# Kernel tuning notes

Measured on AMD Instinct MI355X. Metric: run time of the kernel, lower is better.

## Reference

```python
import jax, jax.numpy as jnp
import numpy as np

N, E, DIN, DOUT, H = 50000, 800000, 256, 128, 8
DH = DOUT // H  # per-head dim = 16


def setup_inputs() -> dict:
    key = jax.random.key(0)
    k1, k2, k3, k4, k5 = jax.random.split(key, 5)
    x = jax.random.normal(k1, (N, DIN), dtype=jnp.float32)
    edge_index = jax.random.randint(k2, (2, E), 0, N)
    W_trans = jax.random.normal(k3, (DOUT, DIN), dtype=jnp.float32) / np.sqrt(DIN).astype(np.float32)
    W_att = jax.random.normal(k4, (1, 2 * DH), dtype=jnp.float32) / np.sqrt(2 * DH).astype(np.float32)
    b_att = jax.random.normal(k5, (1,), dtype=jnp.float32) * 0.01
    return {"x": x, "W_trans": W_trans, "W_att": W_att, "b_att": b_att, "edge_index": edge_index}


def reference(x, W_trans, W_att, b_att, edge_index):
    n = x.shape[0]
    # append self-loops (as in the torch module)
    loops = jnp.arange(n, dtype=edge_index.dtype)
    ei = jnp.concatenate([edge_index, jnp.stack([loops, loops])], axis=1)  # [2, E+N]
    src, dst = ei[0], ei[1]

    # linear transform, split heads: [n, H, DH]
    h = (x @ W_trans.T).reshape(n, H, DH)
    h_i = h[src]  # [Etot, H, DH]
    h_j = h[dst]  # [Etot, H, DH]

    # per-edge attention score: concat -> linear -> leaky_relu(0.2)
    s = jnp.concatenate([h_i, h_j], axis=-1) @ W_att.T + b_att  # [Etot, H, 1]
    s = jnp.where(s >= 0, s, 0.2 * s)

    # softmax(dim=0)*exp_sum/scatter_add(exp) == exp(s)/segment_sum(exp(s)) per dst node
    e = jnp.exp(s)
    denom = jax.ops.segment_sum(e, dst, num_segments=n)  # [n, H, 1]
    att = e / denom[dst]

    out = jax.ops.segment_sum(h_i * att, dst, num_segments=n)  # [n, H, DH]
    return out.reshape(n, DOUT)  # head_fusion='cat'
```

## Files before the change

kernel.cpp:

```cpp
#include <hip/hip_runtime.h>


constexpr int DIN  = 256;
constexpr int DOUT = 128;
constexpr int H    = 8;
constexpr int CAP  = 5120;
constexpr int CHUNK = 1024;

typedef __attribute__((ext_vector_type(8))) short bf16x8;
typedef __attribute__((ext_vector_type(4))) float f32x4;

__device__ __forceinline__ float lrelu(float s) { return s >= 0.0f ? s : 0.2f * s; }

__device__ __forceinline__ unsigned short f2bf(float f) {
  unsigned u = __float_as_uint(f);
  u += 0x7FFF + ((u >> 16) & 1);
  return (unsigned short)(u >> 16);
}
__device__ __forceinline__ float bflo(unsigned u) { return __uint_as_float(u << 16); }
__device__ __forceinline__ float bfhi(unsigned u) { return __uint_as_float(u & 0xFFFF0000u); }

__device__ __forceinline__ int wave_incl_scan(int v, int lane) {
#pragma unroll
  for (int d = 1; d < 64; d <<= 1) {
    int t = __shfl_up(v, d, 64);
    if (lane >= d) v += t;
  }
  return v;
}

__global__ void conv_w(const float* __restrict__ W, unsigned short* __restrict__ Wbf,
                       int n, int* __restrict__ bcount, int nb) {
  int i = blockIdx.x * blockDim.x + threadIdx.x;
  if (i < n) Wbf[i] = f2bf(W[i]);
  if (blockIdx.x == 0 && threadIdx.x < nb) bcount[threadIdx.x] = 0;
}

__global__ __launch_bounds__(256) void bp_gemm(const float* __restrict__ x,
                                               const unsigned short* __restrict__ Wbf,
                                               unsigned short* __restrict__ hbf, int N,
                                               const int* __restrict__ ei,
                                               int* __restrict__ bcount,
                                               unsigned* __restrict__ pair_buf,
                                               int E, int nb, int bp_blocks) {
  __shared__ int hist[256];
  __shared__ int gbase[256];
  if ((int)blockIdx.x < bp_blocks) {
    int c0 = blockIdx.x * CHUNK;
    hist[threadIdx.x] = 0;
    __syncthreads();
    int dcache[4];
#pragma unroll
    for (int q = 0; q < 4; ++q) {
      int e = c0 + q * 256 + threadIdx.x;
      dcache[q] = (e < E) ? ei[E + e] : -1;
      if (dcache[q] >= 0) atomicAdd(&hist[dcache[q] >> 8], 1);
    }
    __syncthreads();
    if (threadIdx.x < nb) {
      int c = hist[threadIdx.x];
      gbase[threadIdx.x] = c ? atomicAdd(&bcount[threadIdx.x], c) : 0;
    }
    __syncthreads();
    hist[threadIdx.x] = 0;
    __syncthreads();
#pragma unroll
    for (int q = 0; q < 4; ++q) {
      int e = c0 + q * 256 + threadIdx.x;
      if (dcache[q] >= 0) {
        int s = ei[e];
        int bk = dcache[q] >> 8;
        int r = atomicAdd(&hist[bk], 1);
        pair_buf[bk * CAP + gbase[bk] + r] = ((unsigned)s << 8) | (unsigned)(dcache[q] & 255);
      }
    }
    return;
  }
  int gb = blockIdx.x - bp_blocks;
  int tid = threadIdx.x;
  int w = tid >> 6, lane = tid & 63;
  int mr = lane & 15, kg = lane >> 4;
  int m0 = gb * 32 + (w >> 1) * 16;
  int nt0 = (w & 1) * 4;
  if (m0 >= N) return;
  int rr = m0 + mr;
  if (rr >= N) rr = N - 1;
  const float* xrow = x + (size_t)rr * DIN + kg * 8;

  float4 xa[8], xc[8];
#pragma unroll
  for (int ks = 0; ks < 8; ++ks) {
    xa[ks] = *(const float4*)(xrow + ks * 32);
    xc[ks] = *(const float4*)(xrow + ks * 32 + 4);
  }

  f32x4 acc[4];
#pragma unroll
  for (int t = 0; t < 4; ++t) acc[t] = (f32x4){0.f, 0.f, 0.f, 0.f};

#pragma unroll
  for (int ks = 0; ks < 8; ++ks) {
    bf16x8 a;
    a[0] = (short)f2bf(xa[ks].x); a[1] = (short)f2bf(xa[ks].y);
    a[2] = (short)f2bf(xa[ks].z); a[3] = (short)f2bf(xa[ks].w);
    a[4] = (short)f2bf(xc[ks].x); a[5] = (short)f2bf(xc[ks].y);
    a[6] = (short)f2bf(xc[ks].z); a[7] = (short)f2bf(xc[ks].w);
#pragma unroll
    for (int t = 0; t < 4; ++t) {
      bf16x8 b = *(const bf16x8*)(Wbf + ((nt0 + t) * 16 + mr) * DIN + ks * 32 + kg * 8);
      acc[t] = __builtin_amdgcn_mfma_f32_16x16x32_bf16(a, b, acc[t], 0, 0, 0);
    }
  }
#pragma unroll
  for (int t = 0; t < 4; ++t) {
#pragma unroll
    for (int r = 0; r < 4; ++r) {
      int row = m0 + kg * 4 + r;
      if (row < N) hbf[row * DOUT + (nt0 + t) * 16 + mr] = f2bf(acc[t][r]);
    }
  }
}

__global__ __launch_bounds__(256) void fs_ns(const unsigned* __restrict__ pair_buf,
                                             const int* __restrict__ bcount,
                                             int* __restrict__ offsets,
                                             unsigned short* __restrict__ src_sorted,
                                             const unsigned short* __restrict__ hbf,
                                             const float* __restrict__ Wa,
                                             float* __restrict__ a_src,
                                             float* __restrict__ a_dst,
                                             int N, int E, int nb) {
  __shared__ int cnt[256];
  __shared__ int cur[256];
  __shared__ int redS[256];
  __shared__ int wsumS[4];
  const int t = threadIdx.x;
  if ((int)blockIdx.x >= nb) {
    int idx = ((int)blockIdx.x - nb) * 256 + t;
    if (idx >= N * H) return;
    int v = idx >> 3, hh = idx & 7;
    const unsigned short* hp = hbf + (size_t)v * DOUT + hh * 16;
    uint4 p0 = *(const uint4*)hp;
    uint4 p1 = *(const uint4*)(hp + 8);
    float hv[16];
    hv[0] = bflo(p0.x); hv[1] = bfhi(p0.x); hv[2] = bflo(p0.y); hv[3] = bfhi(p0.y);
    hv[4] = bflo(p0.z); hv[5] = bfhi(p0.z); hv[6] = bflo(p0.w); hv[7] = bfhi(p0.w);
    hv[8] = bflo(p1.x); hv[9] = bfhi(p1.x); hv[10] = bflo(p1.y); hv[11] = bfhi(p1.y);
    hv[12] = bflo(p1.z); hv[13] = bfhi(p1.z); hv[14] = bflo(p1.w); hv[15] = bfhi(p1.w);
    float s1 = 0.f, s2 = 0.f;
#pragma unroll
    for (int d = 0; d < 16; ++d) {
      s1 += hv[d] * Wa[d];
      s2 += hv[d] * Wa[16 + d];
    }
    a_src[idx] = s1;
    a_dst[idx] = s2;
    return;
  }
  const int B = blockIdx.x;
  const int node0 = B * 256;
  const int v = node0 + t;
  const int valid = (v < N);
  cnt[t] = valid ? 1 : 0;
  __syncthreads();
  const int cntE = bcount[B];
  const unsigned* reg = pair_buf + B * CAP;
  for (int i = t; i < cntE; i += 256)
    atomicAdd(&cnt[reg[i] & 255], 1);
  redS[t] = (t < B) ? bcount[t] : 0;
  __syncthreads();
  for (int s = 128; s > 0; s >>= 1) {
    if (t < s) redS[t] += redS[t + s];
    __syncthreads();
  }
  const int csr_base = redS[0] + node0;
  int val = cnt[t];
  int lane = t & 63, wv = t >> 6;
  int inc = wave_incl_scan(val, lane);
  if (lane == 63) wsumS[wv] = inc;
  __syncthreads();
  int base = 0;
  for (int q = 0; q < wv; ++q) base += wsumS[q];
  int ex = base + inc - val;
  cur[t] = ex + 1;
  if (valid) {
    offsets[v] = csr_base + ex;
    src_sorted[csr_base + ex] = (unsigned short)v;
  }
  if (B == 0 && t == 0) offsets[N] = E + N;
  __syncthreads();
  for (int i = t; i < cntE; i += 256) {
    unsigned p = reg[i];
    int k = atomicAdd(&cur[p & 255], 1);
    src_sorted[csr_base + k] = (unsigned short)(p >> 8);
  }
}

__global__ __launch_bounds__(256) void aggregate(const unsigned short* __restrict__ hbf,
                                                 const float* __restrict__ a_src,
                                                 const float* __restrict__ a_dst,
                                                 const float* __restrict__ b_att,
                                                 const int* __restrict__ offsets,
                                                 const unsigned short* __restrict__ src_sorted,
                                                 float* __restrict__ out, int N) {
  int wid = blockIdx.x * 4 + (threadIdx.x >> 6);
  if (wid >= N) return;
  int lane = threadIdx.x & 63;
  int g = lane >> 4, sl = lane & 15;
  int head = sl >> 1;
  float adv = a_dst[wid * H + head] + b_att[0];
  int beg = offsets[wid], end = offsets[wid + 1];
  float a0 = 0, a1 = 0, a2 = 0, a3 = 0, a4 = 0, a5 = 0, a6 = 0, a7 = 0, den = 0;
  for (int j0 = beg; j0 < end; j0 += 4) {
    int jj = j0 + g;
    bool valid = jj < end;
    int jc = valid ? jj : beg;
    int s = src_sorted[jc];
    float as = a_src[s * H + head];
    uint4 u = *(const uint4*)(hbf + s * DOUT + sl * 8);
    float e = valid ? __expf(lrelu(as + adv)) : 0.f;
    den += e;
    a0 += e * bflo(u.x); a1 += e * bfhi(u.x);
    a2 += e * bflo(u.y); a3 += e * bfhi(u.y);
    a4 += e * bflo(u.z); a5 += e * bfhi(u.z);
    a6 += e * bflo(u.w); a7 += e * bfhi(u.w);
  }
  den += __shfl_xor(den, 16, 64); den += __shfl_xor(den, 32, 64);
  a0 += __shfl_xor(a0, 16, 64); a0 += __shfl_xor(a0, 32, 64);
  a1 += __shfl_xor(a1, 16, 64); a1 += __shfl_xor(a1, 32, 64);
  a2 += __shfl_xor(a2, 16, 64); a2 += __shfl_xor(a2, 32, 64);
  a3 += __shfl_xor(a3, 16, 64); a3 += __shfl_xor(a3, 32, 64);
  a4 += __shfl_xor(a4, 16, 64); a4 += __shfl_xor(a4, 32, 64);
  a5 += __shfl_xor(a5, 16, 64); a5 += __shfl_xor(a5, 32, 64);
  a6 += __shfl_xor(a6, 16, 64); a6 += __shfl_xor(a6, 32, 64);
  a7 += __shfl_xor(a7, 16, 64); a7 += __shfl_xor(a7, 32, 64);
  float inv = 1.0f / den;
  if (g == 0) {
    float4 o = make_float4(a0 * inv, a1 * inv, a2 * inv, a3 * inv);
    *(float4*)&out[wid * DOUT + sl * 8] = o;
  } else if (g == 1) {
    float4 o = make_float4(a4 * inv, a5 * inv, a6 * inv, a7 * inv);
    *(float4*)&out[wid * DOUT + sl * 8 + 4] = o;
  }
}

extern "C" void kernel_launch(void* const* d_in, const int* in_sizes, int n_in,
                              void* d_out, int out_size, void* d_ws, size_t ws_size,
                              hipStream_t stream) {
  const float* x     = (const float*)d_in[0];
  const float* W     = (const float*)d_in[1];
  const float* Wa    = (const float*)d_in[2];
  const float* b_att = (const float*)d_in[3];
  const int*   ei    = (const int*)d_in[4];
  const int N  = in_sizes[0] / DIN;
  const int E  = in_sizes[4] / 2;
  const int NB = (N + 255) / 256;
  float* out = (float*)d_out;

  char* p = (char*)d_ws;
  auto take = [&p](size_t bytes) {
    uintptr_t u = ((uintptr_t)p + 15) & ~(uintptr_t)15;
    p = (char*)(u + bytes);
    return (void*)u;
  };
  unsigned short* hbf = (unsigned short*)take((size_t)N * DOUT * 2);
  unsigned short* Wbf = (unsigned short*)take((size_t)DOUT * DIN * 2);
  float* a_src        = (float*)take((size_t)N * H * 4);
  float* a_dst        = (float*)take((size_t)N * H * 4);
  int* bcount         = (int*)take((size_t)NB * 4);
  unsigned* pair_buf  = (unsigned*)take((size_t)NB * CAP * 4);
  int* offsets        = (int*)take((size_t)(N + 1) * 4);
  unsigned short* src_sorted = (unsigned short*)take((size_t)(E + N + 16) * 2);

  dim3 b256(256);
  const int bp_blocks   = (E + CHUNK - 1) / CHUNK;
  const int gemm_blocks = (N + 31) / 32;
  const int ns_blocks   = (N * H + 255) / 256;

  conv_w<<<dim3((DOUT * DIN + 255) / 256), b256, 0, stream>>>(W, Wbf, DOUT * DIN, bcount, NB);
  bp_gemm<<<dim3(bp_blocks + gemm_blocks), b256, 0, stream>>>(
      x, Wbf, hbf, N, ei, bcount, pair_buf, E, NB, bp_blocks);
  fs_ns<<<dim3(NB + ns_blocks), b256, 0, stream>>>(
      pair_buf, bcount, offsets, src_sorted, hbf, Wa, a_src, a_dst, N, E, NB);
  aggregate<<<dim3((N + 3) / 4), b256, 0, stream>>>(hbf, a_src, a_dst, b_att, offsets,
                                                    src_sorted, out, N);
}
```

Before: 202.5 us.

## Drop weight-conversion kernel, convert W inline, enlarge bucket chunks, reorder fused blocks

Removes the separate conv_w launch: the GEMM now reads fp32 W directly and converts it to bf16 in registers, and the bucket counters are cleared with hipMemsetAsync instead. The edge-bucketing chunk grows from 1024 to 4096 edges per block, which cuts the number of global atomics on bucket counts. Block order in the fused kernels is swapped so GEMM blocks and node-score blocks are dispatched first. The trade-off is twice the W bytes loaded per GEMM block, extra conversion ALU work, and fewer, larger bucketing blocks that hold more registers.

```diff
diff --git a/kernel.cpp b/kernel.cpp
--- a/kernel.cpp
+++ b/kernel.cpp
@@ -1,11 +1,12 @@
 #include <hip/hip_runtime.h>
+#include <string.h>
 
 
 constexpr int DIN  = 256;
 constexpr int DOUT = 128;
 constexpr int H    = 8;
 constexpr int CAP  = 5120;
-constexpr int CHUNK = 1024;
+constexpr int CHUNK = 4096;
 
 typedef __attribute__((ext_vector_type(8))) short bf16x8;
 typedef __attribute__((ext_vector_type(4))) float f32x4;
@@ -29,29 +30,31 @@
   return v;
 }
 
-__global__ void conv_w(const float* __restrict__ W, unsigned short* __restrict__ Wbf,
-                       int n, int* __restrict__ bcount, int nb) {
-  int i = blockIdx.x * blockDim.x + threadIdx.x;
-  if (i < n) Wbf[i] = f2bf(W[i]);
-  if (blockIdx.x == 0 && threadIdx.x < nb) bcount[threadIdx.x] = 0;
-}
-
-__global__ __launch_bounds__(256) void bp_gemm(const float* __restrict__ x,
-                                               const unsigned short* __restrict__ Wbf,
+__device__ __forceinline__ bf16x8 pack8(const float4& lo, const float4& hi) {
+  bf16x8 a;
+  a[0] = (short)f2bf(lo.x); a[1] = (short)f2bf(lo.y);
+  a[2] = (short)f2bf(lo.z); a[3] = (short)f2bf(lo.w);
+  a[4] = (short)f2bf(hi.x); a[5] = (short)f2bf(hi.y);
+  a[6] = (short)f2bf(hi.z); a[7] = (short)f2bf(hi.w);
+  return a;
+}
+
+__global__ __launch_bounds__(256) void gemm_bp(const float* __restrict__ x,
+                                               const float* __restrict__ W,
                                                unsigned short* __restrict__ hbf, int N,
                                                const int* __restrict__ ei,
                                                int* __restrict__ bcount,
                                                unsigned* __restrict__ pair_buf,
-                                               int E, int nb, int bp_blocks) {
+                                               int E, int nb, int gemm_blocks) {
   __shared__ int hist[256];
   __shared__ int gbase[256];
-  if ((int)blockIdx.x < bp_blocks) {
-    int c0 = blockIdx.x * CHUNK;
+  if ((int)blockIdx.x >= gemm_blocks) {
+    int c0 = (blockIdx.x - gemm_blocks) * CHUNK;
     hist[threadIdx.x] = 0;
     __syncthreads();
-    int dcache[4];
-#pragma unroll
-    for (int q = 0; q < 4; ++q) {
+    int dcache[16];
+#pragma unroll
+    for (int q = 0; q < 16; ++q) {
       int e = c0 + q * 256 + threadIdx.x;
       dcache[q] = (e < E) ? ei[E + e] : -1;
       if (dcache[q] >= 0) atomicAdd(&hist[dcache[q] >> 8], 1);
@@ -65,7 +68,7 @@
     hist[threadIdx.x] = 0;
     __syncthreads();
 #pragma unroll
-    for (int q = 0; q < 4; ++q) {
+    for (int q = 0; q < 16; ++q) {
       int e = c0 + q * 256 + threadIdx.x;
       if (dcache[q] >= 0) {
         int s = ei[e];
@@ -76,7 +79,7 @@
     }
     return;
   }
-  int gb = blockIdx.x - bp_blocks;
+  int gb = blockIdx.x;
   int tid = threadIdx.x;
   int w = tid >> 6, lane = tid & 63;
   int mr = lane & 15, kg = lane >> 4;
@@ -100,14 +103,13 @@
 
 #pragma unroll
   for (int ks = 0; ks < 8; ++ks) {
-    bf16x8 a;
-    a[0] = (short)f2bf(xa[ks].x); a[1] = (short)f2bf(xa[ks].y);
-    a[2] = (short)f2bf(xa[ks].z); a[3] = (short)f2bf(xa[ks].w);
-    a[4] = (short)f2bf(xc[ks].x); a[5] = (short)f2bf(xc[ks].y);
-    a[6] = (short)f2bf(xc[ks].z); a[7] = (short)f2bf(xc[ks].w);
+    bf16x8 a = pack8(xa[ks], xc[ks]);
 #pragma unroll
     for (int t = 0; t < 4; ++t) {
-      bf16x8 b = *(const bf16x8*)(Wbf + ((nt0 + t) * 16 + mr) * DIN + ks * 32 + kg * 8);
+      const float* wp = W + ((nt0 + t) * 16 + mr) * DIN + ks * 32 + kg * 8;
+      float4 blo = *(const float4*)wp;
+      float4 bhi = *(const float4*)(wp + 4);
+      bf16x8 b = pack8(blo, bhi);
       acc[t] = __builtin_amdgcn_mfma_f32_16x16x32_bf16(a, b, acc[t], 0, 0, 0);
     }
   }
@@ -121,7 +123,7 @@
   }
 }
 
-__global__ __launch_bounds__(256) void fs_ns(const unsigned* __restrict__ pair_buf,
+__global__ __launch_bounds__(256) void ns_fs(const unsigned* __restrict__ pair_buf,
                                              const int* __restrict__ bcount,
                                              int* __restrict__ offsets,
                                              unsigned short* __restrict__ src_sorted,
@@ -129,14 +131,14 @@
                                              const float* __restrict__ Wa,
                                              float* __restrict__ a_src,
                                              float* __restrict__ a_dst,
-                                             int N, int E, int nb) {
+                                             int N, int E, int nb, int ns_blocks) {
   __shared__ int cnt[256];
   __shared__ int cur[256];
   __shared__ int redS[256];
   __shared__ int wsumS[4];
   const int t = threadIdx.x;
-  if ((int)blockIdx.x >= nb) {
-    int idx = ((int)blockIdx.x - nb) * 256 + t;
+  if ((int)blockIdx.x < ns_blocks) {
+    int idx = (int)blockIdx.x * 256 + t;
     if (idx >= N * H) return;
     int v = idx >> 3, hh = idx & 7;
     const unsigned short* hp = hbf + (size_t)v * DOUT + hh * 16;
@@ -157,7 +159,7 @@
     a_dst[idx] = s2;
     return;
   }
-  const int B = blockIdx.x;
+  const int B = blockIdx.x - ns_blocks;
   const int node0 = B * 256;
   const int v = node0 + t;
   const int valid = (v < N);
@@ -264,7 +266,6 @@
     return (void*)u;
   };
   unsigned short* hbf = (unsigned short*)take((size_t)N * DOUT * 2);
-  unsigned short* Wbf = (unsigned short*)take((size_t)DOUT * DIN * 2);
   float* a_src        = (float*)take((size_t)N * H * 4);
   float* a_dst        = (float*)take((size_t)N * H * 4);
   int* bcount         = (int*)take((size_t)NB * 4);
@@ -273,15 +274,15 @@
   unsigned short* src_sorted = (unsigned short*)take((size_t)(E + N + 16) * 2);
 
   dim3 b256(256);
+  const int gemm_blocks = (N + 31) / 32;
   const int bp_blocks   = (E + CHUNK - 1) / CHUNK;
-  const int gemm_blocks = (N + 31) / 32;
   const int ns_blocks   = (N * H + 255) / 256;
 
-  conv_w<<<dim3((DOUT * DIN + 255) / 256), b256, 0, stream>>>(W, Wbf, DOUT * DIN, bcount, NB);
-  bp_gemm<<<dim3(bp_blocks + gemm_blocks), b256, 0, stream>>>(
-      x, Wbf, hbf, N, ei, bcount, pair_buf, E, NB, bp_blocks);
-  fs_ns<<<dim3(NB + ns_blocks), b256, 0, stream>>>(
-      pair_buf, bcount, offsets, src_sorted, hbf, Wa, a_src, a_dst, N, E, NB);
+  hipMemsetAsync(bcount, 0, (size_t)NB * 4, stream);
+  gemm_bp<<<dim3(gemm_blocks + bp_blocks), b256, 0, stream>>>(
+      x, W, hbf, N, ei, bcount, pair_buf, E, NB, gemm_blocks);
+  ns_fs<<<dim3(ns_blocks + NB), b256, 0, stream>>>(
+      pair_buf, bcount, offsets, src_sorted, hbf, Wa, a_src, a_dst, N, E, NB, ns_blocks);
   aggregate<<<dim3((N + 3) / 4), b256, 0, stream>>>(hbf, a_src, a_dst, b_att, offsets,
                                                     src_sorted, out, N);
 }
```

Result: slower. 209.6 us (+3.5%).
